# Kernel tuning notes

Measured on AMD Instinct MI355X. Metric: run time of the kernel, lower is better.

## Reference

```python
import jax, jax.numpy as jnp
import numpy as np
from jax import lax

BITW = 1
BITA = 3


def _ste_round(x, n):
    # round with straight-through gradient (Round -> Identity override)
    return x + lax.stop_gradient(jnp.round(x * n) / n - x)


def _quantize_active(x, bitA):
    # cabs: clip |x| to [0, 1], then k-bit uniform quantization with STE round
    x = jnp.minimum(1.0, jnp.abs(x))
    if bitA == 32:
        return x
    n = float(2 ** bitA - 1)
    return _ste_round(x, n)


def _quantize_weight(w, bitW):
    if bitW == 32:
        return w
    if bitW == 1:
        # sign with STE (Sign -> Identity): grad w.r.t. w is 1
        E = lax.stop_gradient(jnp.mean(jnp.abs(w)))
        y = w / E
        return (y + lax.stop_gradient(jnp.sign(y) - y)) * E
    n = float(2 ** bitW - 1)
    w = jnp.clip(w * 0.5 + 0.5, 0.0, 1.0)
    return 2.0 * _ste_round(w, n) - 1.0


def setup_inputs() -> dict:
    key = jax.random.key(0)
    kx, kw, kb = jax.random.split(key, 3)
    x = jax.random.normal(kx, (32, 56, 56, 256), dtype=jnp.float32)
    W = jax.random.normal(kw, (3, 3, 256, 256), dtype=jnp.float32) * 0.02  # HWIO
    b = jax.random.normal(kb, (256,), dtype=jnp.float32) * 0.01
    return {"x": x, "W": W, "b": b}


def reference(x, W, b):
    xq = _quantize_active(x, BITA)          # [N,H,W,C] quantized activations
    wq = _quantize_weight(W, BITW)          # [kh,kw,Cin,Cout] binarized weights
    out = lax.conv_general_dilated(
        xq, wq,
        window_strides=(1, 1),
        padding="SAME",
        dimension_numbers=("NHWC", "HWIO", "NHWC"),
    )
    return out + b  # act = identity
```

## Files before the change

kernel.cpp:

```cpp
#include <hip/hip_runtime.h>

typedef __attribute__((ext_vector_type(4))) int int4v;
typedef __attribute__((ext_vector_type(16))) int int16v;

#define NPIX 100352
#define PPIX 107648
#define KTAP 2304
#define CHB (PPIX * 16)
#define LDB 272
#define BTILE (128 * LDB)

__global__ __launch_bounds__(256) void quant_w_kernel(const float* __restrict__ Wm,
                                                      signed char* __restrict__ Bt,
                                                      float* __restrict__ Esum) {
  __shared__ signed char sT[64][80];
  __shared__ float red[4];
  const int k0 = blockIdx.x * 64;
  const int c0 = blockIdx.y * 64;
  const int t = threadIdx.x;
  const int cc = t & 63;
  const int r0 = (t >> 6) * 16;
  float s = 0.f;
#pragma unroll
  for (int i = 0; i < 16; ++i) {
    const int k = r0 + i;
    float w = Wm[(long)(k0 + k) * 256 + c0 + cc];
    s += fabsf(w);
    sT[cc][k] = (signed char)((w > 0.f) ? 1 : ((w < 0.f) ? -1 : 0));
  }
#pragma unroll
  for (int o = 32; o > 0; o >>= 1) s += __shfl_down(s, o, 64);
  if ((t & 63) == 0) red[t >> 6] = s;
  __syncthreads();
  if (t == 0) atomicAdd(Esum, red[0] + red[1] + red[2] + red[3]);
  const int co = t >> 2;
  const int kc = (t & 3) * 16;
  int4v v = *(const int4v*)&sT[co][kc];
  *(int4v*)(Bt + (long)(c0 + co) * KTAP + k0 + kc) = v;
}

__global__ __launch_bounds__(256) void quant_x_kernel(const float* __restrict__ x,
                                                      signed char* __restrict__ xqT) {
  const int tid = blockIdx.x * 256 + threadIdx.x;
  float4 v = ((const float4*)x)[tid];
  unsigned q;
  q  = (unsigned)(int)rintf(fminf(1.f, fabsf(v.x)) * 7.f);
  q |= ((unsigned)(int)rintf(fminf(1.f, fabsf(v.y)) * 7.f)) << 8;
  q |= ((unsigned)(int)rintf(fminf(1.f, fabsf(v.z)) * 7.f)) << 16;
  q |= ((unsigned)(int)rintf(fminf(1.f, fabsf(v.w)) * 7.f)) << 24;
  const int pix = tid >> 6;
  const int l = tid & 63;
  const int n = pix / 3136;
  const int rem = pix - n * 3136;
  const int h = rem / 56, w = rem - (rem / 56) * 56;
  const int pp = (n * 58 + h + 1) * 58 + (w + 1);
  const int c = l >> 2, j = l & 3;
  *(unsigned*)(xqT + (long)c * CHB + pp * 16 + j * 4) = q;
}

__global__ __launch_bounds__(256, 3) void conv_kernel(const signed char* __restrict__ xqT,
                                                      const signed char* __restrict__ Bt,
                                                      const float* __restrict__ bias,
                                                      const float* __restrict__ Esum,
                                                      float* __restrict__ out) {
  __shared__ signed char Bs[BTILE];

  const int t = threadIdx.x;
  const int lane = t & 63;
  const int wid = t >> 6;
  const int bid = blockIdx.x;
  const int tile = (bid & 7) * 196 + (bid >> 3);
  const int m0 = (tile >> 1) * 128;
  const int n0 = (tile & 1) * 128;
  const int wm = (wid & 1) * 64;
  const int wn = (wid >> 1) * 64;
  const int lrow = lane & 31;
  const int half = lane >> 5;

  const signed char *ap0, *ap1;
  {
    const int p0 = m0 + wm + lrow;
    const int n_ = p0 / 3136, r_ = p0 - n_ * 3136;
    const int h_ = r_ / 56, w_ = r_ - h_ * 56;
    ap0 = xqT + (long)half * CHB + ((n_ * 58 + h_ + 1) * 58 + (w_ + 1)) * 16;
    const int p1 = p0 + 32;
    const int n2 = p1 / 3136, r2 = p1 - n2 * 3136;
    const int h2 = r2 / 56, w2 = r2 - h2 * 56;
    ap1 = xqT + (long)half * CHB + ((n2 * 58 + h2 + 1) * 58 + (w2 + 1)) * 16;
  }
  auto dp16 = [](int tap) { return ((tap / 3 - 1) * 58 + (tap % 3) - 1) * 16; };

  const int brow = t >> 4;
  const int bcol = (t & 15) * 16;
  const int gb0 = (n0 + brow) * KTAP + bcol;
  const int lb0 = brow * LDB + bcol;

  int16v acc[2][2];
#pragma unroll
  for (int a = 0; a < 2; ++a)
#pragma unroll
    for (int b = 0; b < 2; ++b)
#pragma unroll
      for (int r = 0; r < 16; ++r) acc[a][b][r] = 0;

  int4v rb[8];
#pragma unroll
  for (int i = 0; i < 8; ++i) rb[i] = *(const int4v*)(Bt + gb0 + i * (16 * KTAP));
  int4v raA0 = *(const int4v*)(ap0 + dp16(0));
  int4v raA1 = *(const int4v*)(ap1 + dp16(0));

  for (int s = 0; s < 9; ++s) {
    if (s) __builtin_amdgcn_s_barrier();
#pragma unroll
    for (int i = 0; i < 8; ++i) *(int4v*)(Bs + lb0 + i * (16 * LDB)) = rb[i];
    asm volatile("s_waitcnt lgkmcnt(0)" ::: "memory");
    __builtin_amdgcn_sched_barrier(0);
    __builtin_amdgcn_s_barrier();
    __builtin_amdgcn_sched_barrier(0);

    if (s + 1 < 9) {
      const int go = (s + 1) * 256;
#pragma unroll
      for (int i = 0; i < 8; ++i)
        rb[i] = *(const int4v*)(Bt + gb0 + go + i * (16 * KTAP));
    }

    const signed char* a0s = ap0 + dp16(s);
    const signed char* a1s = ap1 + dp16(s);
    const int dnx = dp16(s + 1 < 9 ? s + 1 : s);

#pragma unroll
    for (int ks = 0; ks < 8; ++ks) {
      int4v nx0 = *(const int4v*)((ks < 7) ? (a0s + (ks + 1) * (2 * CHB))
                                           : (ap0 + dnx));
      int4v nx1 = *(const int4v*)((ks < 7) ? (a1s + (ks + 1) * (2 * CHB))
                                           : (ap1 + dnx));
      const int ko = ks * 32 + half * 16;
      int4v b0 = *(const int4v*)(Bs + (wn + lrow) * LDB + ko);
      int4v b1 = *(const int4v*)(Bs + (wn + 32 + lrow) * LDB + ko);
      __builtin_amdgcn_s_setprio(1);
      acc[0][0] = __builtin_amdgcn_mfma_i32_32x32x32_i8(raA0, b0, acc[0][0], 0, 0, 0);
      acc[0][1] = __builtin_amdgcn_mfma_i32_32x32x32_i8(raA0, b1, acc[0][1], 0, 0, 0);
      acc[1][0] = __builtin_amdgcn_mfma_i32_32x32x32_i8(raA1, b0, acc[1][0], 0, 0, 0);
      acc[1][1] = __builtin_amdgcn_mfma_i32_32x32x32_i8(raA1, b1, acc[1][1], 0, 0, 0);
      __builtin_amdgcn_s_setprio(0);
      raA0 = nx0; raA1 = nx1;
    }
  }

  const float scale = Esum[0] * (1.0f / (589824.0f * 7.0f));
#pragma unroll
  for (int mt = 0; mt < 2; ++mt)
#pragma unroll
    for (int nt = 0; nt < 2; ++nt) {
      const int col = n0 + wn + nt * 32 + lrow;
      const float bv = bias[col];
#pragma unroll
      for (int r = 0; r < 16; ++r) {
        const int row = (r & 3) + 8 * (r >> 2) + 4 * half;
        const int m = m0 + wm + mt * 32 + row;
        out[(long)m * 256 + col] = (float)acc[mt][nt][r] * scale + bv;
      }
    }
}

extern "C" void kernel_launch(void* const* d_in, const int* in_sizes, int n_in,
                              void* d_out, int out_size, void* d_ws, size_t ws_size,
                              hipStream_t stream) {
  const float* x    = (const float*)d_in[0];
  const float* Wm   = (const float*)d_in[1];
  const float* bias = (const float*)d_in[2];
  float* out = (float*)d_out;

  float* Esum = (float*)d_ws;
  signed char* Bt  = (signed char*)d_ws + 256;
  signed char* xqT = (signed char*)d_ws + 256 + 589824;

  hipMemsetAsync(d_ws, 0, 4, stream);
  hipMemsetAsync(xqT, 0, 27557888, stream);
  quant_w_kernel<<<dim3(36, 4), 256, 0, stream>>>(Wm, Bt, Esum);
  quant_x_kernel<<<25088, 256, 0, stream>>>(x, xqT);
  conv_kernel<<<1568, 256, 0, stream>>>(xqT, Bt, bias, Esum, out);
}
```

Baseline: 252.0 us.

## Halve conv N-tile to 64, deepen A/B register prefetch, raise occupancy

Shrinks each conv block's output tile from 128x128 to 128x64, so each wave computes a 64x32 sub-tile with two MFMA accumulators instead of four. The grid doubles to 3136 blocks, the LDS B tile halves, and launch bounds target 4 blocks per CU. A loads now run three k-steps ahead through a 4-deep register ring, and B fragments are read from LDS two steps ahead through a 3-deep ring. In exchange, A-operand reuse per loaded fragment is halved, so global and L2 traffic for activations roughly doubles.

```diff
diff --git a/kernel.cpp b/kernel.cpp
--- a/kernel.cpp
+++ b/kernel.cpp
@@ -8,7 +8,7 @@
 #define KTAP 2304
 #define CHB (PPIX * 16)
 #define LDB 272
-#define BTILE (128 * LDB)
+#define BTILE (64 * LDB)
 
 __global__ __launch_bounds__(256) void quant_w_kernel(const float* __restrict__ Wm,
                                                       signed char* __restrict__ Bt,
@@ -58,7 +58,7 @@
   *(unsigned*)(xqT + (long)c * CHB + pp * 16 + j * 4) = q;
 }
 
-__global__ __launch_bounds__(256, 3) void conv_kernel(const signed char* __restrict__ xqT,
+__global__ __launch_bounds__(256, 4) void conv_kernel(const signed char* __restrict__ xqT,
                                                       const signed char* __restrict__ Bt,
                                                       const float* __restrict__ bias,
                                                       const float* __restrict__ Esum,
@@ -69,11 +69,11 @@
   const int lane = t & 63;
   const int wid = t >> 6;
   const int bid = blockIdx.x;
-  const int tile = (bid & 7) * 196 + (bid >> 3);
-  const int m0 = (tile >> 1) * 128;
-  const int n0 = (tile & 1) * 128;
+  const int tile = (bid & 7) * 392 + (bid >> 3);
+  const int m0 = (tile >> 2) * 128;
+  const int n0 = (tile & 3) * 64;
   const int wm = (wid & 1) * 64;
-  const int wn = (wid >> 1) * 64;
+  const int wn = (wid >> 1) * 32;
   const int lrow = lane & 31;
   const int half = lane >> 5;
 
@@ -92,76 +92,86 @@
 
   const int brow = t >> 4;
   const int bcol = (t & 15) * 16;
-  const int gb0 = (n0 + brow) * KTAP + bcol;
-  const int lb0 = brow * LDB + bcol;
+  const int gbB = (n0 + brow) * KTAP + bcol;
+  const int lbw = brow * LDB + bcol;
+  const signed char* brd = Bs + (wn + lrow) * LDB + half * 16;
 
-  int16v acc[2][2];
+  int16v acc0, acc1;
 #pragma unroll
-  for (int a = 0; a < 2; ++a)
+  for (int r = 0; r < 16; ++r) { acc0[r] = 0; acc1[r] = 0; }
+
+  int4v rb[4];
 #pragma unroll
-    for (int b = 0; b < 2; ++b)
+  for (int i = 0; i < 4; ++i) rb[i] = *(const int4v*)(Bt + gbB + i * (16 * KTAP));
+  int4v ra0[4], ra1[4], bf[3];
+  {
+    const signed char* p0 = ap0 + dp16(0);
+    const signed char* p1 = ap1 + dp16(0);
 #pragma unroll
-      for (int r = 0; r < 16; ++r) acc[a][b][r] = 0;
+    for (int j = 0; j < 3; ++j) {
+      ra0[j] = *(const int4v*)(p0 + j * (2 * CHB));
+      ra1[j] = *(const int4v*)(p1 + j * (2 * CHB));
+    }
+  }
 
-  int4v rb[8];
-#pragma unroll
-  for (int i = 0; i < 8; ++i) rb[i] = *(const int4v*)(Bt + gb0 + i * (16 * KTAP));
-  int4v raA0 = *(const int4v*)(ap0 + dp16(0));
-  int4v raA1 = *(const int4v*)(ap1 + dp16(0));
+#define ITER(ks)                                                                  \
+  {                                                                               \
+        \
+    const signed char* pa0 =                                                      \
+        ((ks) + 3 < 8) ? (a0s + ((ks) + 3) * (2 * CHB)) : (a0n + ((ks) - 5) * (2 * CHB)); \
+    const signed char* pa1 =                                                      \
+        ((ks) + 3 < 8) ? (a1s + ((ks) + 3) * (2 * CHB)) : (a1n + ((ks) - 5) * (2 * CHB)); \
+    ra0[((ks) + 3) & 3] = *(const int4v*)pa0;                                     \
+    ra1[((ks) + 3) & 3] = *(const int4v*)pa1;                                     \
+                            \
+    if ((ks) + 2 < 8) bf[((ks) + 2) % 3] = *(const int4v*)(brd + ((ks) + 2) * 32); \
+    __builtin_amdgcn_s_setprio(1);                                                \
+    acc0 = __builtin_amdgcn_mfma_i32_32x32x32_i8(ra0[(ks) & 3], bf[(ks) % 3], acc0, 0, 0, 0); \
+    acc1 = __builtin_amdgcn_mfma_i32_32x32x32_i8(ra1[(ks) & 3], bf[(ks) % 3], acc1, 0, 0, 0); \
+    __builtin_amdgcn_s_setprio(0);                                                \
+  }
 
   for (int s = 0; s < 9; ++s) {
     if (s) __builtin_amdgcn_s_barrier();
 #pragma unroll
-    for (int i = 0; i < 8; ++i) *(int4v*)(Bs + lb0 + i * (16 * LDB)) = rb[i];
+    for (int i = 0; i < 4; ++i) *(int4v*)(Bs + lbw + i * (16 * LDB)) = rb[i];
     asm volatile("s_waitcnt lgkmcnt(0)" ::: "memory");
     __builtin_amdgcn_sched_barrier(0);
     __builtin_amdgcn_s_barrier();
     __builtin_amdgcn_sched_barrier(0);
 
-    if (s + 1 < 9) {
+    if (s < 8) {
       const int go = (s + 1) * 256;
 #pragma unroll
-      for (int i = 0; i < 8; ++i)
-        rb[i] = *(const int4v*)(Bt + gb0 + go + i * (16 * KTAP));
+      for (int i = 0; i < 4; ++i)
+        rb[i] = *(const int4v*)(Bt + gbB + go + i * (16 * KTAP));
     }
 
     const signed char* a0s = ap0 + dp16(s);
     const signed char* a1s = ap1 + dp16(s);
-    const int dnx = dp16(s + 1 < 9 ? s + 1 : s);
+    const signed char* a0n = ap0 + dp16(s < 8 ? s + 1 : 8);
+    const signed char* a1n = ap1 + dp16(s < 8 ? s + 1 : 8);
 
-#pragma unroll
-    for (int ks = 0; ks < 8; ++ks) {
-      int4v nx0 = *(const int4v*)((ks < 7) ? (a0s + (ks + 1) * (2 * CHB))
-                                           : (ap0 + dnx));
-      int4v nx1 = *(const int4v*)((ks < 7) ? (a1s + (ks + 1) * (2 * CHB))
-                                           : (ap1 + dnx));
-      const int ko = ks * 32 + half * 16;
-      int4v b0 = *(const int4v*)(Bs + (wn + lrow) * LDB + ko);
-      int4v b1 = *(const int4v*)(Bs + (wn + 32 + lrow) * LDB + ko);
-      __builtin_amdgcn_s_setprio(1);
-      acc[0][0] = __builtin_amdgcn_mfma_i32_32x32x32_i8(raA0, b0, acc[0][0], 0, 0, 0);
-      acc[0][1] = __builtin_amdgcn_mfma_i32_32x32x32_i8(raA0, b1, acc[0][1], 0, 0, 0);
-      acc[1][0] = __builtin_amdgcn_mfma_i32_32x32x32_i8(raA1, b0, acc[1][0], 0, 0, 0);
-      acc[1][1] = __builtin_amdgcn_mfma_i32_32x32x32_i8(raA1, b1, acc[1][1], 0, 0, 0);
-      __builtin_amdgcn_s_setprio(0);
-      raA0 = nx0; raA1 = nx1;
-    }
+    bf[0] = *(const int4v*)(brd);
+    bf[1] = *(const int4v*)(brd + 32);
+
+    ITER(0) ITER(1) ITER(2) ITER(3) ITER(4) ITER(5) ITER(6) ITER(7)
   }
+#undef ITER
 
   const float scale = Esum[0] * (1.0f / (589824.0f * 7.0f));
+  const int col = n0 + wn + lrow;
+  const float bv = bias[col];
 #pragma unroll
-  for (int mt = 0; mt < 2; ++mt)
+  for (int r = 0; r < 16; ++r) {
+    const int row = (r & 3) + 8 * (r >> 2) + 4 * half;
+    out[(long)(m0 + wm + row) * 256 + col] = (float)acc0[r] * scale + bv;
+  }
 #pragma unroll
-    for (int nt = 0; nt < 2; ++nt) {
-      const int col = n0 + wn + nt * 32 + lrow;
-      const float bv = bias[col];
-#pragma unroll
-      for (int r = 0; r < 16; ++r) {
-        const int row = (r & 3) + 8 * (r >> 2) + 4 * half;
-        const int m = m0 + wm + mt * 32 + row;
-        out[(long)m * 256 + col] = (float)acc[mt][nt][r] * scale + bv;
-      }
-    }
+  for (int r = 0; r < 16; ++r) {
+    const int row = (r & 3) + 8 * (r >> 2) + 4 * half;
+    out[(long)(m0 + wm + 32 + row) * 256 + col] = (float)acc1[r] * scale + bv;
+  }
 }
 
 extern "C" void kernel_launch(void* const* d_in, const int* in_sizes, int n_in,
@@ -180,5 +190,5 @@
   hipMemsetAsync(xqT, 0, 27557888, stream);
   quant_w_kernel<<<dim3(36, 4), 256, 0, stream>>>(Wm, Bt, Esum);
   quant_x_kernel<<<25088, 256, 0, stream>>>(x, xqT);
-  conv_kernel<<<1568, 256, 0, stream>>>(xqT, Bt, bias, Esum, out);
+  conv_kernel<<<3136, 256, 0, stream>>>(xqT, Bt, bias, Esum, out);
 }
```

Result: slower. 261.9 us (+4.0%).
